# Kernel optimization log

Measured on AMD Instinct MI355X. Metric: run time of the kernel, lower is better.

The kernel has to match this reference:

```python
import jax, jax.numpy as jnp
import numpy as np

LENGTHSCALE = 1.0


def setup_inputs() -> dict:
    key = jax.random.key(0)
    k1, k2, k3 = jax.random.split(key, 3)
    M, N, D = 4096, 8192, 256
    X = jax.random.normal(k1, (M, D), dtype=jnp.float32)
    X_train = jax.random.normal(k2, (N, D), dtype=jnp.float32)
    alpha = jax.random.normal(k3, (N, 1), dtype=jnp.float32)
    return {"X": X, "X_train": X_train, "alpha": alpha}


def _rbf_kernel(X1, X2, lengthscale=LENGTHSCALE):
    # Same math as sum((X1[:,None]-X2[None,:])**2, -1) without the [M,N,D] tensor.
    sq1 = jnp.sum(X1 * X1, axis=-1, keepdims=True)          # [M,1]
    sq2 = jnp.sum(X2 * X2, axis=-1)                         # [N]
    dist_sq = sq1 + sq2[None, :] - 2.0 * (X1 @ X2.T)        # [M,N]
    return jnp.exp(-dist_sq / (2.0 * lengthscale ** 2))


def reference(X, X_train, alpha):
    K_star = _rbf_kernel(X, X_train)    # [M,N]
    pred = K_star @ alpha               # [M,1]
    return pred
```

## Files before the change

kernel.cpp:

```cpp
#include <hip/hip_runtime.h>
#include <hip/hip_bf16.h>

#define M_DIM 4096
#define N_DIM 8192
#define D_DIM 256
#define NSLICE 32
#define NCHUNK 16
#define C_EXP (-0.7213475204444817f)
#define K_ACC (1.4426950408889634f)
#define SKIP_THR (-151.0f)
#define BUFB 8192
#define SQAL_OFF (4 * BUFB)
#define LDS_BYTES (4 * BUFB + 2048)

typedef __attribute__((ext_vector_type(8))) short short8;
typedef __attribute__((ext_vector_type(4))) float f32x4;

__device__ inline unsigned short f2bf(float f) {
    __hip_bfloat16 h = __float2bfloat16(f);
    return *reinterpret_cast<unsigned short*>(&h);
}

__global__ __launch_bounds__(256) void prep_kernel(
    const float* __restrict__ X, const float* __restrict__ T,
    const float* __restrict__ alpha,
    unsigned short* __restrict__ Xb, unsigned short* __restrict__ Tb,
    float* __restrict__ sq1, float2* __restrict__ sqal)
{
    const int row  = blockIdx.x * 4 + (threadIdx.x >> 6);
    const int lane = threadIdx.x & 63;
    const float* src; unsigned short* dst; int r; bool isX;
    if (row < M_DIM) { src = X; dst = Xb; r = row; isX = true; }
    else             { src = T; dst = Tb; r = row - M_DIM; isX = false; }

    const float4* s4 = reinterpret_cast<const float4*>(src + (size_t)r * D_DIM);
    float4 v = s4[lane];
    float ss = v.x * v.x + v.y * v.y + v.z * v.z + v.w * v.w;

    ushort4 b4;
    b4.x = f2bf(v.x); b4.y = f2bf(v.y); b4.z = f2bf(v.z); b4.w = f2bf(v.w);
    reinterpret_cast<ushort4*>(dst + (size_t)r * D_DIM)[lane] = b4;

    #pragma unroll
    for (int o = 1; o < 64; o <<= 1) ss += __shfl_xor(ss, o);
    if (lane == 0) {
        if (isX) sq1[r] = ss * C_EXP;
        else     sqal[r] = make_float2(ss * C_EXP, alpha[r]);
    }
}

__global__ __launch_bounds__(256, 2) void gemm_kernel(
    const unsigned short* __restrict__ Xb, const unsigned short* __restrict__ Tb,
    const float* __restrict__ sq1, const float2* __restrict__ sqal,
    float* __restrict__ part)
{
    __shared__ __align__(16) char smem[LDS_BYTES];
    const int cslice = blockIdx.x & 31;
    const int quad   = blockIdx.x >> 5;
    const int wid    = threadIdx.x >> 6;
    const int lane   = threadIdx.x & 63;
    const int l15    = lane & 15;
    const int lg     = lane >> 4;

    const int rowbase = quad * 256 + wid * 64;
    const int colbase = cslice * 256;

    short8 af[4][8];
    #pragma unroll
    for (int m = 0; m < 4; ++m)
        #pragma unroll
        for (int ks = 0; ks < 8; ++ks)
            af[m][ks] = *(const short8*)(Xb +
                (size_t)(rowbase + m * 16 + l15) * D_DIM + ks * 32 + lg * 8);

    float4 s1v[4];
    #pragma unroll
    for (int m = 0; m < 4; ++m)
        s1v[m] = *reinterpret_cast<const float4*>(sq1 + rowbase + m * 16 + lg * 4);
    float s1max = -1e30f;
    #pragma unroll
    for (int m = 0; m < 4; ++m)
        #pragma unroll
        for (int r = 0; r < 4; ++r) s1max = fmaxf(s1max, s1v[m][r]);

    asm volatile("s_waitcnt vmcnt(0)" ::: "memory");

    const char* TbB = (const char*)Tb;
    const char* SaB = (const char*)sqal + (size_t)colbase * 8;

    #pragma unroll
    for (int s = 0; s < 2; ++s)
        __builtin_amdgcn_global_load_lds(
            (const __attribute__((address_space(1))) void*)(SaB + s * 1024 + lane * 16),
            (__attribute__((address_space(3))) void*)(smem + SQAL_OFF + s * 1024), 16, 0, 0);

    auto stage = [&](int i) {
        char* buf = smem + (i & 3) * BUFB;
        #pragma unroll
        for (int c = 0; c < 2; ++c) {
            const int j = wid * 2 + c;
            const int col_local = j * 2 + (lane >> 5);
            const size_t src = (size_t)(colbase + i * 16 + col_local) * 512
                             + (size_t)((((lane & 31) ^ (col_local & 7)) * 16));
            __builtin_amdgcn_global_load_lds(
                (const __attribute__((address_space(1))) void*)(TbB + src),
                (__attribute__((address_space(3))) void*)(buf + j * 1024), 16, 0, 0);
        }
    };

    float psum[4][4];
    #pragma unroll
    for (int m = 0; m < 4; ++m)
        #pragma unroll
        for (int r = 0; r < 4; ++r) psum[m][r] = 0.0f;

    auto compute = [&](int i) {
        const char* buf = smem + (i & 3) * BUFB;
        f32x4 acc[4];
        #pragma unroll
        for (int m = 0; m < 4; ++m) acc[m] = (f32x4)0.0f;
        #pragma unroll
        for (int ks = 0; ks < 8; ++ks) {
            const short8 bf = *(const short8*)(buf + l15 * 512 +
                (((ks * 4 + lg) ^ (l15 & 7)) * 16));
            #pragma unroll
            for (int m = 0; m < 4; ++m)
                acc[m] = __builtin_amdgcn_mfma_f32_16x16x32_bf16(
                    af[m][ks], bf, acc[m], 0, 0, 0);
        }
        const float2 sa = *(const float2*)(smem + SQAL_OFF + (i * 16 + l15) * 8);
        float amax = acc[0][0];
        #pragma unroll
        for (int m = 0; m < 4; ++m)
            #pragma unroll
            for (int r = 0; r < 4; ++r) amax = fmaxf(amax, acc[m][r]);
        const float bound = fmaf(amax, K_ACC, s1max + sa.x);
        if (!__all(bound < SKIP_THR)) {
            #pragma unroll
            for (int m = 0; m < 4; ++m)
                #pragma unroll
                for (int r = 0; r < 4; ++r) {
                    const float arg = fmaf(acc[m][r], K_ACC, s1v[m][r] + sa.x);
                    psum[m][r] = fmaf(__builtin_amdgcn_exp2f(arg), sa.y, psum[m][r]);
                }
        }
    };

    stage(0);
    stage(1);
    #pragma unroll
    for (int i = 0; i < NCHUNK; ++i) {
        if (i + 2 < NCHUNK) {
            stage(i + 2);
            asm volatile("s_waitcnt vmcnt(4)" ::: "memory");
        } else if (i + 1 < NCHUNK) {
            asm volatile("s_waitcnt vmcnt(2)" ::: "memory");
        } else {
            asm volatile("s_waitcnt vmcnt(0)" ::: "memory");
        }
        __builtin_amdgcn_s_barrier();
        compute(i);
    }

    #pragma unroll
    for (int m = 0; m < 4; ++m) {
        float4 pv;
        #pragma unroll
        for (int r = 0; r < 4; ++r) {
            float p = psum[m][r];
            p += __shfl_xor(p, 1);
            p += __shfl_xor(p, 2);
            p += __shfl_xor(p, 4);
            p += __shfl_xor(p, 8);
            ((float*)&pv)[r] = p;
        }
        if (l15 == 0)
            *reinterpret_cast<float4*>(part + (size_t)cslice * M_DIM +
                                       rowbase + m * 16 + lg * 4) = pv;
    }
}

__global__ __launch_bounds__(256) void reduce_kernel(
    const float* __restrict__ part, float* __restrict__ out)
{
    const int gi = blockIdx.x * 256 + threadIdx.x;
    float s = 0.0f;
    #pragma unroll
    for (int b = 0; b < NSLICE; ++b) s += part[(size_t)b * M_DIM + gi];
    out[gi] = s;
}

extern "C" void kernel_launch(void* const* d_in, const int* in_sizes, int n_in,
                              void* d_out, int out_size, void* d_ws, size_t ws_size,
                              hipStream_t stream)
{
    const float* X  = (const float*)d_in[0];
    const float* T  = (const float*)d_in[1];
    const float* al = (const float*)d_in[2];
    float* out = (float*)d_out;

    char* ws = (char*)d_ws;
    unsigned short* Xb = (unsigned short*)ws;
    unsigned short* Tb = (unsigned short*)(ws + (size_t)M_DIM * D_DIM * 2);
    float* sq1  = (float*)(ws + (size_t)(M_DIM + N_DIM) * D_DIM * 2);
    float2* sqal = (float2*)(sq1 + M_DIM);
    float* part = (float*)(sqal + N_DIM);

    prep_kernel<<<(M_DIM + N_DIM) / 4, 256, 0, stream>>>(X, T, al, Xb, Tb, sq1, sqal);
    gemm_kernel<<<16 * NSLICE, 256, 0, stream>>>(Xb, Tb, sq1, sqal, part);
    reduce_kernel<<<M_DIM / 256, 256, 0, stream>>>(part, out);
}
```

Before: 34.45 us.

## Use 8 waves per block with smaller row tiles and deeper prefetch

Splits each block's 256 rows across 8 waves of 32 rows instead of 4 waves of 64, halving per-wave accumulators and A-fragment registers to raise occupancy. It also increases the LDS ring to 8 buffers and prefetches 4 chunks ahead, with one load per wave per stage. In exchange, each LDS B-fragment read feeds only two MFMAs, so LDS traffic per FLOP doubles. LDS use per block also roughly doubles.

```diff
diff --git a/kernel.cpp b/kernel.cpp
--- a/kernel.cpp
+++ b/kernel.cpp
@@ -6,12 +6,13 @@
 #define D_DIM 256
 #define NSLICE 32
 #define NCHUNK 16
+#define LOOKAHEAD 4
 #define C_EXP (-0.7213475204444817f)
 #define K_ACC (1.4426950408889634f)
 #define SKIP_THR (-151.0f)
 #define BUFB 8192
-#define SQAL_OFF (4 * BUFB)
-#define LDS_BYTES (4 * BUFB + 2048)
+#define SQAL_OFF (8 * BUFB)
+#define LDS_BYTES (8 * BUFB + 2048)
 
 typedef __attribute__((ext_vector_type(8))) short short8;
 typedef __attribute__((ext_vector_type(4))) float f32x4;
@@ -49,7 +50,7 @@
     }
 }
 
-__global__ __launch_bounds__(256, 2) void gemm_kernel(
+__global__ __launch_bounds__(512, 4) void gemm_kernel(
     const unsigned short* __restrict__ Xb, const unsigned short* __restrict__ Tb,
     const float* __restrict__ sq1, const float2* __restrict__ sqal,
     float* __restrict__ part)
@@ -62,24 +63,24 @@
     const int l15    = lane & 15;
     const int lg     = lane >> 4;
 
-    const int rowbase = quad * 256 + wid * 64;
+    const int rowbase = quad * 256 + wid * 32;
     const int colbase = cslice * 256;
 
-    short8 af[4][8];
-    #pragma unroll
-    for (int m = 0; m < 4; ++m)
+    short8 af[2][8];
+    #pragma unroll
+    for (int m = 0; m < 2; ++m)
         #pragma unroll
         for (int ks = 0; ks < 8; ++ks)
             af[m][ks] = *(const short8*)(Xb +
                 (size_t)(rowbase + m * 16 + l15) * D_DIM + ks * 32 + lg * 8);
 
-    float4 s1v[4];
-    #pragma unroll
-    for (int m = 0; m < 4; ++m)
+    float4 s1v[2];
+    #pragma unroll
+    for (int m = 0; m < 2; ++m)
         s1v[m] = *reinterpret_cast<const float4*>(sq1 + rowbase + m * 16 + lg * 4);
     float s1max = -1e30f;
     #pragma unroll
-    for (int m = 0; m < 4; ++m)
+    for (int m = 0; m < 2; ++m)
         #pragma unroll
         for (int r = 0; r < 4; ++r) s1max = fmaxf(s1max, s1v[m][r]);
 
@@ -95,49 +96,42 @@
             (__attribute__((address_space(3))) void*)(smem + SQAL_OFF + s * 1024), 16, 0, 0);
 
     auto stage = [&](int i) {
-        char* buf = smem + (i & 3) * BUFB;
-        #pragma unroll
-        for (int c = 0; c < 2; ++c) {
-            const int j = wid * 2 + c;
-            const int col_local = j * 2 + (lane >> 5);
-            const size_t src = (size_t)(colbase + i * 16 + col_local) * 512
-                             + (size_t)((((lane & 31) ^ (col_local & 7)) * 16));
-            __builtin_amdgcn_global_load_lds(
-                (const __attribute__((address_space(1))) void*)(TbB + src),
-                (__attribute__((address_space(3))) void*)(buf + j * 1024), 16, 0, 0);
-        }
+        char* buf = smem + (i & 7) * BUFB;
+        const int col_local = wid * 2 + (lane >> 5);
+        const size_t src = (size_t)(colbase + i * 16 + col_local) * 512
+                         + (size_t)(((lane & 31) ^ (col_local & 7)) * 16);
+        __builtin_amdgcn_global_load_lds(
+            (const __attribute__((address_space(1))) void*)(TbB + src),
+            (__attribute__((address_space(3))) void*)(buf + wid * 1024), 16, 0, 0);
     };
 
-    float psum[4][4];
-    #pragma unroll
-    for (int m = 0; m < 4; ++m)
+    float psum[2][4];
+    #pragma unroll
+    for (int m = 0; m < 2; ++m)
         #pragma unroll
         for (int r = 0; r < 4; ++r) psum[m][r] = 0.0f;
 
     auto compute = [&](int i) {
-        const char* buf = smem + (i & 3) * BUFB;
-        f32x4 acc[4];
-        #pragma unroll
-        for (int m = 0; m < 4; ++m) acc[m] = (f32x4)0.0f;
+        const char* buf = smem + (i & 7) * BUFB;
+        f32x4 acc[2];
+        acc[0] = (f32x4)0.0f; acc[1] = (f32x4)0.0f;
         #pragma unroll
         for (int ks = 0; ks < 8; ++ks) {
             const short8 bf = *(const short8*)(buf + l15 * 512 +
                 (((ks * 4 + lg) ^ (l15 & 7)) * 16));
-            #pragma unroll
-            for (int m = 0; m < 4; ++m)
-                acc[m] = __builtin_amdgcn_mfma_f32_16x16x32_bf16(
-                    af[m][ks], bf, acc[m], 0, 0, 0);
+            acc[0] = __builtin_amdgcn_mfma_f32_16x16x32_bf16(af[0][ks], bf, acc[0], 0, 0, 0);
+            acc[1] = __builtin_amdgcn_mfma_f32_16x16x32_bf16(af[1][ks], bf, acc[1], 0, 0, 0);
         }
         const float2 sa = *(const float2*)(smem + SQAL_OFF + (i * 16 + l15) * 8);
         float amax = acc[0][0];
         #pragma unroll
-        for (int m = 0; m < 4; ++m)
+        for (int m = 0; m < 2; ++m)
             #pragma unroll
             for (int r = 0; r < 4; ++r) amax = fmaxf(amax, acc[m][r]);
         const float bound = fmaf(amax, K_ACC, s1max + sa.x);
         if (!__all(bound < SKIP_THR)) {
             #pragma unroll
-            for (int m = 0; m < 4; ++m)
+            for (int m = 0; m < 2; ++m)
                 #pragma unroll
                 for (int r = 0; r < 4; ++r) {
                     const float arg = fmaf(acc[m][r], K_ACC, s1v[m][r] + sa.x);
@@ -146,15 +140,19 @@
         }
     };
 
-    stage(0);
-    stage(1);
+    #pragma unroll
+    for (int i = 0; i < LOOKAHEAD; ++i) stage(i);
     #pragma unroll
     for (int i = 0; i < NCHUNK; ++i) {
-        if (i + 2 < NCHUNK) {
-            stage(i + 2);
+        if (i + LOOKAHEAD < NCHUNK) {
+            stage(i + LOOKAHEAD);
             asm volatile("s_waitcnt vmcnt(4)" ::: "memory");
+        } else if (i + 3 < NCHUNK) {
+            asm volatile("s_waitcnt vmcnt(3)" ::: "memory");
+        } else if (i + 2 < NCHUNK) {
+            asm volatile("s_waitcnt vmcnt(2)" ::: "memory");
         } else if (i + 1 < NCHUNK) {
-            asm volatile("s_waitcnt vmcnt(2)" ::: "memory");
+            asm volatile("s_waitcnt vmcnt(1)" ::: "memory");
         } else {
             asm volatile("s_waitcnt vmcnt(0)" ::: "memory");
         }
@@ -163,7 +161,7 @@
     }
 
     #pragma unroll
-    for (int m = 0; m < 4; ++m) {
+    for (int m = 0; m < 2; ++m) {
         float4 pv;
         #pragma unroll
         for (int r = 0; r < 4; ++r) {
@@ -207,6 +205,6 @@
     float* part = (float*)(sqal + N_DIM);
 
     prep_kernel<<<(M_DIM + N_DIM) / 4, 256, 0, stream>>>(X, T, al, Xb, Tb, sq1, sqal);
-    gemm_kernel<<<16 * NSLICE, 256, 0, stream>>>(Xb, Tb, sq1, sqal, part);
+    gemm_kernel<<<16 * NSLICE, 512, 0, stream>>>(Xb, Tb, sq1, sqal, part);
     reduce_kernel<<<M_DIM / 256, 256, 0, stream>>>(part, out);
 }
```

Result: no change. 34.50 us (+0.1%).

## Restructure GEMM into 256x256 tiles staging both operands through LDS with 8 waves

Applied to the files above, without the earlier changes.

The GEMM kernel now uses 512 threads per block (8 waves arranged 2x4), each computing a 128x64 output sub-tile. Both X and T tiles are staged through a 128KB double-buffered LDS with swizzled global_load_lds over four 64-wide K steps, replacing the register-resident A fragments and the stream of 16-column B chunks. The exp and alpha epilogue now runs once after the full K loop, and per-wave partial sums are combined in LDS before being written out. The aim is more MFMA reuse per loaded byte and better overlap via setprio and barriers. The cost is heavy register pressure from 32 accumulators, 128KB of LDS (which limits occupancy), and a skip test that is coarser because it now covers a whole tile.

```diff
diff --git a/kernel.cpp b/kernel.cpp
--- a/kernel.cpp
+++ b/kernel.cpp
@@ -5,13 +5,12 @@
 #define N_DIM 8192
 #define D_DIM 256
 #define NSLICE 32
-#define NCHUNK 16
 #define C_EXP (-0.7213475204444817f)
 #define K_ACC (1.4426950408889634f)
 #define SKIP_THR (-151.0f)
-#define BUFB 8192
-#define SQAL_OFF (4 * BUFB)
-#define LDS_BYTES (4 * BUFB + 2048)
+
+#define AS1 __attribute__((address_space(1)))
+#define AS3 __attribute__((address_space(3)))
 
 typedef __attribute__((ext_vector_type(8))) short short8;
 typedef __attribute__((ext_vector_type(4))) float f32x4;
@@ -49,121 +48,196 @@
     }
 }
 
-__global__ __launch_bounds__(256, 2) void gemm_kernel(
+__global__ __launch_bounds__(512, 2) void gemm_kernel(
     const unsigned short* __restrict__ Xb, const unsigned short* __restrict__ Tb,
     const float* __restrict__ sq1, const float2* __restrict__ sqal,
     float* __restrict__ part)
 {
-    __shared__ __align__(16) char smem[LDS_BYTES];
-    const int cslice = blockIdx.x & 31;
-    const int quad   = blockIdx.x >> 5;
-    const int wid    = threadIdx.x >> 6;
-    const int lane   = threadIdx.x & 63;
-    const int l15    = lane & 15;
-    const int lg     = lane >> 4;
-
-    const int rowbase = quad * 256 + wid * 64;
-    const int colbase = cslice * 256;
-
-    short8 af[4][8];
-    #pragma unroll
-    for (int m = 0; m < 4; ++m)
-        #pragma unroll
-        for (int ks = 0; ks < 8; ++ks)
-            af[m][ks] = *(const short8*)(Xb +
-                (size_t)(rowbase + m * 16 + l15) * D_DIM + ks * 32 + lg * 8);
-
-    float4 s1v[4];
-    #pragma unroll
-    for (int m = 0; m < 4; ++m)
-        s1v[m] = *reinterpret_cast<const float4*>(sq1 + rowbase + m * 16 + lg * 4);
-    float s1max = -1e30f;
-    #pragma unroll
-    for (int m = 0; m < 4; ++m)
-        #pragma unroll
-        for (int r = 0; r < 4; ++r) s1max = fmaxf(s1max, s1v[m][r]);
-
-    asm volatile("s_waitcnt vmcnt(0)" ::: "memory");
-
+    __shared__ __align__(16) char smem[131072];
+    const int bn   = blockIdx.x & 31;
+    const int bm   = blockIdx.x >> 5;
+    const int tid  = threadIdx.x;
+    const int wid  = tid >> 6;
+    const int lane = tid & 63;
+    const int l15  = lane & 15, lg = lane >> 4, xr = l15 & 7;
+    const int wr   = wid >> 2, wc = wid & 3;
+    const int rsub = lane >> 3;
+    const int sg16 = ((lane & 7) ^ rsub) * 16;
+
+    const char* XbB = (const char*)Xb;
     const char* TbB = (const char*)Tb;
-    const char* SaB = (const char*)sqal + (size_t)colbase * 8;
-
-    #pragma unroll
-    for (int s = 0; s < 2; ++s)
-        __builtin_amdgcn_global_load_lds(
-            (const __attribute__((address_space(1))) void*)(SaB + s * 1024 + lane * 16),
-            (__attribute__((address_space(3))) void*)(smem + SQAL_OFF + s * 1024), 16, 0, 0);
-
-    auto stage = [&](int i) {
-        char* buf = smem + (i & 3) * BUFB;
+
+    auto stage2 = [&](int ktn, int p) {
+        if (ktn > 3) return;
         #pragma unroll
         for (int c = 0; c < 2; ++c) {
-            const int j = wid * 2 + c;
-            const int col_local = j * 2 + (lane >> 5);
-            const size_t src = (size_t)(colbase + i * 16 + col_local) * 512
-                             + (size_t)((((lane & 31) ^ (col_local & 7)) * 16));
+            const int g = wid + 8 * (2 * p + c);
+            const int h = g >> 4, blk = g & 15;
+            const int dest = (ktn & 1) * 65536 + (h & 1) * 32768
+                           + (h >> 1) * 16384 + blk * 1024;
+            const char* sb = (h < 2) ? XbB : TbB;
+            const int rc = ((h < 2) ? bm : bn) * 256 + (h & 1) * 128
+                         + blk * 8 + rsub;
+            const size_t src = (size_t)rc * 512 + (size_t)(ktn * 128 + sg16);
             __builtin_amdgcn_global_load_lds(
-                (const __attribute__((address_space(1))) void*)(TbB + src),
-                (__attribute__((address_space(3))) void*)(buf + j * 1024), 16, 0, 0);
+                (const AS1 void*)(sb + src), (AS3 void*)(smem + dest), 16, 0, 0);
         }
     };
 
-    float psum[4][4];
-    #pragma unroll
-    for (int m = 0; m < 4; ++m)
+    f32x4 acc[8][4];
+    #pragma unroll
+    for (int m = 0; m < 8; ++m)
+        #pragma unroll
+        for (int n = 0; n < 4; ++n) acc[m][n] = (f32x4)0.0f;
+
+    #pragma unroll
+    for (int p = 0; p < 4; ++p) stage2(0, p);
+
+    short8 af0[4][2], af1[4][2], bf0[2][2], bf1[2][2];
+
+    #pragma unroll
+    for (int kt = 0; kt < 4; ++kt) {
+        const char* Abase = smem + (kt & 1) * 65536 + wr * 32768;
+        const char* Bbase = smem + (kt & 1) * 65536 + 16384 + (wc >> 1) * 32768
+                          + ((wc & 1) * 64) * 128;
+
+        stage2(kt + 1, 0);
+        if (kt < 3) asm volatile("s_waitcnt vmcnt(2)" ::: "memory");
+        else        asm volatile("s_waitcnt vmcnt(0)" ::: "memory");
+        __builtin_amdgcn_s_barrier();
+        __builtin_amdgcn_sched_barrier(0);
+        #pragma unroll
+        for (int m = 0; m < 4; ++m)
+            #pragma unroll
+            for (int ks = 0; ks < 2; ++ks)
+                af0[m][ks] = *(const short8*)(Abase + (m * 16 + l15) * 128
+                                              + (((ks * 4 + lg) ^ xr)) * 16);
+        #pragma unroll
+        for (int n = 0; n < 2; ++n)
+            #pragma unroll
+            for (int ks = 0; ks < 2; ++ks)
+                bf0[n][ks] = *(const short8*)(Bbase + (n * 16 + l15) * 128
+                                              + (((ks * 4 + lg) ^ xr)) * 16);
+        __builtin_amdgcn_s_setprio(1);
+        #pragma unroll
+        for (int ks = 0; ks < 2; ++ks)
+            #pragma unroll
+            for (int m = 0; m < 4; ++m)
+                #pragma unroll
+                for (int n = 0; n < 2; ++n)
+                    acc[m][n] = __builtin_amdgcn_mfma_f32_16x16x32_bf16(
+                        af0[m][ks], bf0[n][ks], acc[m][n], 0, 0, 0);
+        __builtin_amdgcn_s_setprio(0);
+        __builtin_amdgcn_s_barrier();
+        __builtin_amdgcn_sched_barrier(0);
+
+        stage2(kt + 1, 1);
+        #pragma unroll
+        for (int n = 0; n < 2; ++n)
+            #pragma unroll
+            for (int ks = 0; ks < 2; ++ks)
+                bf1[n][ks] = *(const short8*)(Bbase + (32 + n * 16 + l15) * 128
+                                              + (((ks * 4 + lg) ^ xr)) * 16);
+        __builtin_amdgcn_s_barrier();
+        __builtin_amdgcn_sched_barrier(0);
+        __builtin_amdgcn_s_setprio(1);
+        #pragma unroll
+        for (int ks = 0; ks < 2; ++ks)
+            #pragma unroll
+            for (int m = 0; m < 4; ++m)
+                #pragma unroll
+                for (int n = 0; n < 2; ++n)
+                    acc[m][2 + n] = __builtin_amdgcn_mfma_f32_16x16x32_bf16(
+                        af0[m][ks], bf1[n][ks], acc[m][2 + n], 0, 0, 0);
+        __builtin_amdgcn_s_setprio(0);
+        __builtin_amdgcn_s_barrier();
+        __builtin_amdgcn_sched_barrier(0);
+
+        stage2(kt + 1, 2);
+        #pragma unroll
+        for (int m = 0; m < 4; ++m)
+            #pragma unroll
+            for (int ks = 0; ks < 2; ++ks)
+                af1[m][ks] = *(const short8*)(Abase + (64 + m * 16 + l15) * 128
+                                              + (((ks * 4 + lg) ^ xr)) * 16);
+        __builtin_amdgcn_s_barrier();
+        __builtin_amdgcn_sched_barrier(0);
+        __builtin_amdgcn_s_setprio(1);
+        #pragma unroll
+        for (int ks = 0; ks < 2; ++ks)
+            #pragma unroll
+            for (int m = 0; m < 4; ++m)
+                #pragma unroll
+                for (int n = 0; n < 2; ++n)
+                    acc[4 + m][2 + n] = __builtin_amdgcn_mfma_f32_16x16x32_bf16(
+                        af1[m][ks], bf1[n][ks], acc[4 + m][2 + n], 0, 0, 0);
+        __builtin_amdgcn_s_setprio(0);
+        __builtin_amdgcn_s_barrier();
+        __builtin_amdgcn_sched_barrier(0);
+
+        stage2(kt + 1, 3);
+        __builtin_amdgcn_s_barrier();
+        __builtin_amdgcn_sched_barrier(0);
+        __builtin_amdgcn_s_setprio(1);
+        #pragma unroll
+        for (int ks = 0; ks < 2; ++ks)
+            #pragma unroll
+            for (int m = 0; m < 4; ++m)
+                #pragma unroll
+                for (int n = 0; n < 2; ++n)
+                    acc[4 + m][n] = __builtin_amdgcn_mfma_f32_16x16x32_bf16(
+                        af1[m][ks], bf0[n][ks], acc[4 + m][n], 0, 0, 0);
+        __builtin_amdgcn_s_setprio(0);
+        __builtin_amdgcn_s_barrier();
+        __builtin_amdgcn_sched_barrier(0);
+    }
+
+    const int rowbase = bm * 256 + wr * 128;
+    float4 s1v[8];
+    #pragma unroll
+    for (int m = 0; m < 8; ++m)
+        s1v[m] = *reinterpret_cast<const float4*>(sq1 + rowbase + m * 16 + lg * 4);
+    float2 sa[4];
+    #pragma unroll
+    for (int n = 0; n < 4; ++n)
+        sa[n] = sqal[bn * 256 + wc * 64 + n * 16 + l15];
+
+    float amax = acc[0][0][0], s1m = s1v[0][0], s2m = sa[0].x;
+    #pragma unroll
+    for (int m = 0; m < 8; ++m)
+        #pragma unroll
+        for (int n = 0; n < 4; ++n)
+            #pragma unroll
+            for (int r = 0; r < 4; ++r) amax = fmaxf(amax, acc[m][n][r]);
+    #pragma unroll
+    for (int m = 0; m < 8; ++m)
+        #pragma unroll
+        for (int r = 0; r < 4; ++r) s1m = fmaxf(s1m, s1v[m][r]);
+    #pragma unroll
+    for (int n = 0; n < 4; ++n) s2m = fmaxf(s2m, sa[n].x);
+
+    float psum[8][4];
+    #pragma unroll
+    for (int m = 0; m < 8; ++m)
         #pragma unroll
         for (int r = 0; r < 4; ++r) psum[m][r] = 0.0f;
 
-    auto compute = [&](int i) {
-        const char* buf = smem + (i & 3) * BUFB;
-        f32x4 acc[4];
-        #pragma unroll
-        for (int m = 0; m < 4; ++m) acc[m] = (f32x4)0.0f;
-        #pragma unroll
-        for (int ks = 0; ks < 8; ++ks) {
-            const short8 bf = *(const short8*)(buf + l15 * 512 +
-                (((ks * 4 + lg) ^ (l15 & 7)) * 16));
-            #pragma unroll
-            for (int m = 0; m < 4; ++m)
-                acc[m] = __builtin_amdgcn_mfma_f32_16x16x32_bf16(
-                    af[m][ks], bf, acc[m], 0, 0, 0);
-        }
-        const float2 sa = *(const float2*)(smem + SQAL_OFF + (i * 16 + l15) * 8);
-        float amax = acc[0][0];
-        #pragma unroll
-        for (int m = 0; m < 4; ++m)
-            #pragma unroll
-            for (int r = 0; r < 4; ++r) amax = fmaxf(amax, acc[m][r]);
-        const float bound = fmaf(amax, K_ACC, s1max + sa.x);
-        if (!__all(bound < SKIP_THR)) {
-            #pragma unroll
-            for (int m = 0; m < 4; ++m)
+    const float bound = fmaf(amax, K_ACC, s1m + s2m);
+    if (!__all(bound < SKIP_THR)) {
+        #pragma unroll
+        for (int m = 0; m < 8; ++m)
+            #pragma unroll
+            for (int n = 0; n < 4; ++n)
                 #pragma unroll
                 for (int r = 0; r < 4; ++r) {
-                    const float arg = fmaf(acc[m][r], K_ACC, s1v[m][r] + sa.x);
-                    psum[m][r] = fmaf(__builtin_amdgcn_exp2f(arg), sa.y, psum[m][r]);
+                    const float arg = fmaf(acc[m][n][r], K_ACC, s1v[m][r] + sa[n].x);
+                    psum[m][r] = fmaf(__builtin_amdgcn_exp2f(arg), sa[n].y, psum[m][r]);
                 }
-        }
-    };
-
-    stage(0);
-    stage(1);
-    #pragma unroll
-    for (int i = 0; i < NCHUNK; ++i) {
-        if (i + 2 < NCHUNK) {
-            stage(i + 2);
-            asm volatile("s_waitcnt vmcnt(4)" ::: "memory");
-        } else if (i + 1 < NCHUNK) {
-            asm volatile("s_waitcnt vmcnt(2)" ::: "memory");
-        } else {
-            asm volatile("s_waitcnt vmcnt(0)" ::: "memory");
-        }
-        __builtin_amdgcn_s_barrier();
-        compute(i);
-    }
-
-    #pragma unroll
-    for (int m = 0; m < 4; ++m) {
+    }
+
+    float* red = (float*)smem;
+    #pragma unroll
+    for (int m = 0; m < 8; ++m) {
         float4 pv;
         #pragma unroll
         for (int r = 0; r < 4; ++r) {
@@ -175,8 +249,12 @@
             ((float*)&pv)[r] = p;
         }
         if (l15 == 0)
-            *reinterpret_cast<float4*>(part + (size_t)cslice * M_DIM +
-                                       rowbase + m * 16 + lg * 4) = pv;
+            *reinterpret_cast<float4*>(&red[wc * 256 + wr * 128 + m * 16 + lg * 4]) = pv;
+    }
+    __syncthreads();
+    if (tid < 256) {
+        const float s = red[tid] + red[256 + tid] + red[512 + tid] + red[768 + tid];
+        part[(size_t)bn * M_DIM + bm * 256 + tid] = s;
     }
 }
 
@@ -207,6 +285,6 @@
     float* part = (float*)(sqal + N_DIM);
 
     prep_kernel<<<(M_DIM + N_DIM) / 4, 256, 0, stream>>>(X, T, al, Xb, Tb, sq1, sqal);
-    gemm_kernel<<<16 * NSLICE, 256, 0, stream>>>(Xb, Tb, sq1, sqal, part);
+    gemm_kernel<<<(M_DIM / 256) * NSLICE, 512, 0, stream>>>(Xb, Tb, sq1, sqal, part);
     reduce_kernel<<<M_DIM / 256, 256, 0, stream>>>(part, out);
 }
```

Result: slower. 36.82 us (+6.9%).
